# Kernel tuning notes

Hardware: AMD Instinct MI355X
Metric: run time of the kernel (lower is better)

The kernel has to match this reference:

```python
import jax, jax.numpy as jnp
import numpy as np

FP8_MAX = 448.0  # finfo(float8_e4m3fn).max
EPS = 1e-12
BLK = 128        # weight_block_size = (128, 128); activation group_size = 128


def setup_inputs() -> dict:
    key = jax.random.key(0)
    k1, k2, k3, k4 = jax.random.split(key, 4)
    B, S, H, O = 4, 4096, 2048, 2048
    x = jax.random.normal(k1, (B, S, H), dtype=jnp.float32)
    # fp8 weight: generate, round to e4m3fn grid, store as f32 (values exactly fp8-representable)
    w_raw = jax.random.normal(k2, (O, H), dtype=jnp.float32) * 0.02
    weight = w_raw.astype(jnp.float8_e4m3fn).astype(jnp.float32)
    # per-(128x128)-block weight scales
    weight_scale = jax.random.uniform(k3, (O // BLK, H // BLK), dtype=jnp.float32,
                                      minval=0.001, maxval=0.01)
    bias = jax.random.normal(k4, (O,), dtype=jnp.float32) * 0.01
    return {"x": x, "weight": weight, "weight_scale": weight_scale, "bias": bias}


def reference(x, weight, weight_scale, bias):
    B, S, H = x.shape
    O = weight.shape[0]
    J = H // BLK  # number of activation groups / weight column-blocks
    # per-token-group fp8 quantization (group_size = BLK)
    xg = x.reshape(-1, J, BLK)                                      # [M, J, BLK]
    max_abs = jnp.clip(jnp.max(jnp.abs(xg), axis=-1, keepdims=True), EPS)
    scales = FP8_MAX / max_abs                                      # [M, J, 1]
    xq = jnp.clip(xg * scales, -FP8_MAX, FP8_MAX)
    xq = xq.astype(jnp.float8_e4m3fn).astype(jnp.float32)           # fp8 round-trip
    inv_scale = 1.0 / scales                                        # stored input_scale
    # block-scaled matmul == dequantize both operands then single GEMM
    x_dq = (xq * inv_scale).reshape(-1, H)                          # [M, H]
    w_scale_full = jnp.repeat(jnp.repeat(weight_scale, BLK, axis=0), BLK, axis=1)  # [O, H]
    w_dq = weight * w_scale_full                                    # [O, H]
    y = x_dq @ w_dq.T + bias                                        # [M, O]
    return y.reshape(B, S, O)
```

## Files before the change

kernel.cpp:

```cpp
#include <hip/hip_runtime.h>
#include <cstdint>

#define FP8MAX 448.0f

typedef float f32x4 __attribute__((ext_vector_type(4)));
typedef int   i32x4 __attribute__((ext_vector_type(4)));
typedef int   i32x8 __attribute__((ext_vector_type(8)));

union frag8 { i32x8 v8; i32x4 v4[2]; };

__device__ __forceinline__ void gload_lds16(const void* g, void* l) {
  __builtin_amdgcn_global_load_lds(
      (const __attribute__((address_space(1))) unsigned int*)g,
      (__attribute__((address_space(3))) unsigned int*)l,
      16, 0, 0);
}

__global__ __launch_bounds__(256) void quant_x(const float* __restrict__ x,
                                               uint8_t* __restrict__ xq,
                                               float* __restrict__ sa) {
  const int m = blockIdx.x;
  const int t = threadIdx.x;
  const float* xr = x + (size_t)m * 2048;
  float4 v0 = ((const float4*)xr)[t * 2];
  float4 v1 = ((const float4*)xr)[t * 2 + 1];
  float amax = fmaxf(fmaxf(fmaxf(fabsf(v0.x), fabsf(v0.y)), fmaxf(fabsf(v0.z), fabsf(v0.w))),
                     fmaxf(fmaxf(fabsf(v1.x), fabsf(v1.y)), fmaxf(fabsf(v1.z), fabsf(v1.w))));
  #pragma unroll
  for (int off = 1; off < 16; off <<= 1)
    amax = fmaxf(amax, __shfl_xor(amax, off));
  amax = fmaxf(amax, 1e-12f);
  float s   = FP8MAX / amax;
  float inv = 1.0f / s;
  if ((t & 15) == 0) sa[(size_t)m * 16 + (t >> 4)] = inv;
  float q[8] = {v0.x * s, v0.y * s, v0.z * s, v0.w * s,
                v1.x * s, v1.y * s, v1.z * s, v1.w * s};
  #pragma unroll
  for (int i = 0; i < 8; ++i) q[i] = fminf(fmaxf(q[i], -FP8MAX), FP8MAX);
  union { unsigned long long u; unsigned int w[2]; } pk;
  pk.w[0] = __builtin_amdgcn_cvt_pk_fp8_f32(q[0], q[1], 0, false);
  pk.w[0] = __builtin_amdgcn_cvt_pk_fp8_f32(q[2], q[3], pk.w[0], true);
  pk.w[1] = __builtin_amdgcn_cvt_pk_fp8_f32(q[4], q[5], 0, false);
  pk.w[1] = __builtin_amdgcn_cvt_pk_fp8_f32(q[6], q[7], pk.w[1], true);
  ((unsigned long long*)(xq + (size_t)m * 2048))[t] = pk.u;
}

__global__ __launch_bounds__(256) void conv_w(const float* __restrict__ w,
                                              uint8_t* __restrict__ w8, int n8) {
  int i = blockIdx.x * 256 + threadIdx.x;
  if (i >= n8) return;
  float4 v0 = ((const float4*)w)[i * 2];
  float4 v1 = ((const float4*)w)[i * 2 + 1];
  union { unsigned long long u; unsigned int x[2]; } pk;
  pk.x[0] = __builtin_amdgcn_cvt_pk_fp8_f32(v0.x, v0.y, 0, false);
  pk.x[0] = __builtin_amdgcn_cvt_pk_fp8_f32(v0.z, v0.w, pk.x[0], true);
  pk.x[1] = __builtin_amdgcn_cvt_pk_fp8_f32(v1.x, v1.y, 0, false);
  pk.x[1] = __builtin_amdgcn_cvt_pk_fp8_f32(v1.z, v1.w, pk.x[1], true);
  ((unsigned long long*)w8)[i] = pk.u;
}

#define SAL_STRIDE 264

__global__ __launch_bounds__(512, 2) void gemm_fp8(
    const uint8_t* __restrict__ A, const uint8_t* __restrict__ Bw,
    const float* __restrict__ sa, const float* __restrict__ sb,
    const float* __restrict__ bias, float* __restrict__ out,
    int M, int N, int K) {
  const int J = K >> 7;
  const int nbn = N >> 8;
  int bid = blockIdx.x;
  int nwg = gridDim.x;
  if ((nwg & 7) == 0) {
    int cpx = nwg >> 3;
    bid = (bid & 7) * cpx + (bid >> 3);
  }
  const int bn = bid % nbn;
  const int bm = bid / nbn;
  const int t = threadIdx.x;
  const int lane = t & 63;
  const int w = t >> 6;
  const int wr = w >> 2;
  const int wc = w & 3;
  const int r16 = lane & 15;
  const int kg = lane >> 4;

  __shared__ __align__(16) uint8_t lA[2][256 * 128];
  __shared__ __align__(16) uint8_t lB[2][256 * 128];
  __shared__ __align__(16) float sal[16 * SAL_STRIDE];

  const uint8_t* gA = A + (size_t)bm * 256 * K;
  const uint8_t* gB = Bw + (size_t)bn * 256 * K;

  for (int i = t; i < 256 * 16; i += 512) {
    int row = i >> 4, j = i & 15;
    sal[j * SAL_STRIDE + row] = sa[((size_t)bm * 256 + row) * 16 + j];
  }

  const int rl = t >> 3;
  const int sg = t & 7;

  #define STAGE(ldst, gbase, h_, kt_) do {                                   \
    _Pragma("unroll")                                                        \
    for (int it_ = 0; it_ < 2; ++it_) {                                      \
      int r_ = it_ * 64 + rl;                                                \
      int gr_ = (h_) * 128 + r_;                                             \
      gload_lds16(gbase + (size_t)gr_ * K + ((kt_) << 7) +                   \
                      ((sg ^ (r_ & 7)) << 4),                                \
                  (ldst) + gr_ * 128 + sg * 16);                             \
    } } while (0)

  __syncthreads();

  STAGE(lA[0], gA, 0, 0);
  STAGE(lB[0], gB, 0, 0);
  STAGE(lA[0], gA, 1, 0);
  STAGE(lB[0], gB, 1, 0);
  STAGE(lA[1], gA, 0, 1);
  STAGE(lB[1], gB, 0, 1);

  f32x4 tot[8][4] = {};
  const f32x4 fz = {0.f, 0.f, 0.f, 0.f};
  frag8 av[4], bv[2][2];
  f32x4 scq[4];

  #define BAR1_VM8  do { asm volatile("s_waitcnt vmcnt(8)" ::: "memory");    \
                         __builtin_amdgcn_s_barrier();                       \
                         asm volatile("" ::: "memory"); } while (0)
  #define BAR1      do { __builtin_amdgcn_s_barrier();                       \
                         asm volatile("" ::: "memory"); } while (0)
  #define MID       do { asm volatile("s_waitcnt lgkmcnt(0)" ::: "memory");  \
                         __builtin_amdgcn_sched_barrier(0); } while (0)
  #define BAR2      do { __builtin_amdgcn_s_barrier();                       \
                         asm volatile("" ::: "memory"); } while (0)

  #define READ_A(mg_, buf_) do { _Pragma("unroll")                           \
    for (int i_ = 0; i_ < 4; ++i_) {                                         \
      int row_ = (mg_) * 128 + wr * 64 + i_ * 16 + r16;                      \
      const uint8_t* bp_ = &lA[buf_][row_ * 128];                            \
      int sw_ = (row_ & 7) << 4;                                             \
      av[i_].v4[0] = *(const i32x4*)(bp_ + ((kg * 32) ^ sw_));               \
      av[i_].v4[1] = *(const i32x4*)(bp_ + ((kg * 32 + 16) ^ sw_));          \
    } } while (0)

  #define READ_B(ng_, buf_) do { _Pragma("unroll")                           \
    for (int j_ = 0; j_ < 2; ++j_) {                                         \
      int row_ = (ng_) * 128 + wc * 32 + j_ * 16 + r16;                      \
      const uint8_t* bp_ = &lB[buf_][row_ * 128];                            \
      int sw_ = (row_ & 7) << 4;                                             \
      bv[ng_][j_].v4[0] = *(const i32x4*)(bp_ + ((kg * 32) ^ sw_));          \
      bv[ng_][j_].v4[1] = *(const i32x4*)(bp_ + ((kg * 32 + 16) ^ sw_));     \
    } } while (0)

  #define CALC_SC(mg_, kt_, sbj_) do { _Pragma("unroll")                     \
    for (int i_ = 0; i_ < 4; ++i_) {                                         \
      scq[i_] = (*(const f32x4*)&sal[(kt_) * SAL_STRIDE + (mg_) * 128 +      \
                                     wr * 64 + i_ * 16 + kg * 4]) * (sbj_);  \
    } } while (0)

  #define MFMA8(mg_, ng_) do {                                               \
    __builtin_amdgcn_s_setprio(1);                                           \
    _Pragma("unroll")                                                        \
    for (int i_ = 0; i_ < 4; ++i_) { _Pragma("unroll")                       \
      for (int j_ = 0; j_ < 2; ++j_) {                                       \
        f32x4 p_ = __builtin_amdgcn_mfma_scale_f32_16x16x128_f8f6f4(         \
            av[i_].v8, bv[ng_][j_].v8, fz, 0, 0, 0, 0x7f7f7f7f, 0,           \
            0x7f7f7f7f);                                                     \
        tot[(mg_) * 4 + i_][(ng_) * 2 + j_] += p_ * scq[i_];                 \
      } }                                                                    \
    __builtin_amdgcn_s_setprio(0); } while (0)

  const int KT = K >> 7;
  const int NI = KT >> 1;
  for (int i = 0; i < NI; ++i) {
    const int kt = 2 * i;
    const int kt2 = (kt + 2 < KT) ? kt + 2 : kt + 2 - KT;
    const int kt3 = (kt + 3 < KT) ? kt + 3 : kt + 3 - KT;
    const float sb0  = sb[(bn * 2 + 0) * J + kt];
    const float sb1  = sb[(bn * 2 + 1) * J + kt];
    const float sb0n = sb[(bn * 2 + 0) * J + kt + 1];
    const float sb1n = sb[(bn * 2 + 1) * J + kt + 1];
    BAR1_VM8;
    READ_A(0, 0); READ_B(0, 0); CALC_SC(0, kt, sb0);
    STAGE(lA[1], gA, 1, kt + 1); STAGE(lB[1], gB, 1, kt + 1);
    MID; MFMA8(0, 0); BAR2;
    BAR1_VM8;
    READ_B(1, 0); CALC_SC(0, kt, sb1);
    MID; MFMA8(0, 1); BAR2;
    BAR1;
    READ_A(1, 0); CALC_SC(1, kt, sb0);
    STAGE(lA[0], gA, 0, kt2);
    MID; MFMA8(1, 0); BAR2;
    BAR1;
    CALC_SC(1, kt, sb1);
    STAGE(lB[0], gB, 0, kt2);
    MID; MFMA8(1, 1); BAR2;
    BAR1_VM8;
    READ_A(0, 1); READ_B(0, 1); CALC_SC(0, kt + 1, sb0n);
    STAGE(lA[0], gA, 1, kt2); STAGE(lB[0], gB, 1, kt2);
    MID; MFMA8(0, 0); BAR2;
    BAR1_VM8;
    READ_B(1, 1); CALC_SC(0, kt + 1, sb1n);
    MID; MFMA8(0, 1); BAR2;
    BAR1;
    READ_A(1, 1); CALC_SC(1, kt + 1, sb0n);
    STAGE(lA[1], gA, 0, kt3);
    MID; MFMA8(1, 0); BAR2;
    BAR1;
    CALC_SC(1, kt + 1, sb1n);
    STAGE(lB[1], gB, 0, kt3);
    MID; MFMA8(1, 1); BAR2;
  }
  asm volatile("s_waitcnt vmcnt(0)" ::: "memory");

  #pragma unroll
  for (int ng = 0; ng < 2; ++ng) {
    float bb[2];
    #pragma unroll
    for (int j = 0; j < 2; ++j)
      bb[j] = bias[bn * 256 + ng * 128 + wc * 32 + j * 16 + r16];
    #pragma unroll
    for (int mg = 0; mg < 2; ++mg) {
      #pragma unroll
      for (int i = 0; i < 4; ++i) {
        int row0 = bm * 256 + mg * 128 + wr * 64 + i * 16 + kg * 4;
        #pragma unroll
        for (int r = 0; r < 4; ++r) {
          float* orow = out + (size_t)(row0 + r) * N + bn * 256 + ng * 128 + wc * 32;
          #pragma unroll
          for (int j = 0; j < 2; ++j)
            orow[j * 16 + r16] = tot[mg * 4 + i][ng * 2 + j][r] + bb[j];
        }
      }
    }
  }
}

extern "C" void kernel_launch(void* const* d_in, const int* in_sizes, int n_in,
                              void* d_out, int out_size, void* d_ws, size_t ws_size,
                              hipStream_t stream) {
  const float* x    = (const float*)d_in[0];
  const float* wt   = (const float*)d_in[1];
  const float* wsc  = (const float*)d_in[2];
  const float* bias = (const float*)d_in[3];
  float* out = (float*)d_out;

  const int O = in_sizes[3];
  const int H = in_sizes[1] / O;
  const int M = in_sizes[0] / H;

  uint8_t* xq = (uint8_t*)d_ws;
  uint8_t* w8 = xq + (size_t)M * H;
  float*   sa = (float*)(w8 + (size_t)O * H);

  quant_x<<<M, 256, 0, stream>>>(x, xq, sa);
  int n8 = O * H / 8;
  conv_w<<<(n8 + 255) / 256, 256, 0, stream>>>(wt, w8, n8);
  int grid = (M / 256) * (O / 256);
  gemm_fp8<<<grid, 512, 0, stream>>>(xq, w8, sa, wsc, bias, out, M, O, H);
}
```

Before: 156.0 us.

## Restructure GEMM main-loop barriers and vmcnt waits for finer-grained load tracking

Result: slower. 162.4 us (+4.2%).

```diff
diff --git a/kernel.cpp b/kernel.cpp
--- a/kernel.cpp
+++ b/kernel.cpp
@@ -59,7 +59,7 @@
   ((unsigned long long*)w8)[i] = pk.u;
 }
 
-#define SAL_STRIDE 264
+#define SAL_STRIDE 260
 
 __global__ __launch_bounds__(512, 2) void gemm_fp8(
     const uint8_t* __restrict__ A, const uint8_t* __restrict__ Bw,
@@ -99,7 +99,7 @@
   const int rl = t >> 3;
   const int sg = t & 7;
 
-  #define STAGE(ldst, gbase, h_, kt_) do {                                   \
+  #define STAGE2(ldst, gbase, h_, kt_) do {                                  \
     _Pragma("unroll")                                                        \
     for (int it_ = 0; it_ < 2; ++it_) {                                      \
       int r_ = it_ * 64 + rl;                                                \
@@ -111,27 +111,26 @@
 
   __syncthreads();
 
-  STAGE(lA[0], gA, 0, 0);
-  STAGE(lB[0], gB, 0, 0);
-  STAGE(lA[0], gA, 1, 0);
-  STAGE(lB[0], gB, 1, 0);
-  STAGE(lA[1], gA, 0, 1);
-  STAGE(lB[1], gB, 0, 1);
+  STAGE2(lA[0], gA, 0, 0);
+  STAGE2(lB[0], gB, 0, 0);
+  STAGE2(lA[0], gA, 1, 0);
+  STAGE2(lB[0], gB, 1, 0);
+  STAGE2(lA[1], gA, 0, 1);
+  STAGE2(lB[1], gB, 0, 1);
+  asm volatile("s_waitcnt vmcnt(4)" ::: "memory");
+  __builtin_amdgcn_s_barrier();
+  asm volatile("" ::: "memory");
 
   f32x4 tot[8][4] = {};
   const f32x4 fz = {0.f, 0.f, 0.f, 0.f};
   frag8 av[4], bv[2][2];
   f32x4 scq[4];
 
-  #define BAR1_VM8  do { asm volatile("s_waitcnt vmcnt(8)" ::: "memory");    \
-                         __builtin_amdgcn_s_barrier();                       \
-                         asm volatile("" ::: "memory"); } while (0)
-  #define BAR1      do { __builtin_amdgcn_s_barrier();                       \
+  #define VM(NN)    asm volatile("s_waitcnt vmcnt(" #NN ")" ::: "memory")
+  #define BARN      do { __builtin_amdgcn_s_barrier();                       \
                          asm volatile("" ::: "memory"); } while (0)
   #define MID       do { asm volatile("s_waitcnt lgkmcnt(0)" ::: "memory");  \
                          __builtin_amdgcn_sched_barrier(0); } while (0)
-  #define BAR2      do { __builtin_amdgcn_s_barrier();                       \
-                         asm volatile("" ::: "memory"); } while (0)
 
   #define READ_A(mg_, buf_) do { _Pragma("unroll")                           \
     for (int i_ = 0; i_ < 4; ++i_) {                                         \
@@ -179,36 +178,31 @@
     const float sb1  = sb[(bn * 2 + 1) * J + kt];
     const float sb0n = sb[(bn * 2 + 0) * J + kt + 1];
     const float sb1n = sb[(bn * 2 + 1) * J + kt + 1];
-    BAR1_VM8;
     READ_A(0, 0); READ_B(0, 0); CALC_SC(0, kt, sb0);
-    STAGE(lA[1], gA, 1, kt + 1); STAGE(lB[1], gB, 1, kt + 1);
-    MID; MFMA8(0, 0); BAR2;
-    BAR1_VM8;
+    STAGE2(lA[1], gA, 1, kt + 1); STAGE2(lB[1], gB, 1, kt + 1);
+    BARN; MID; MFMA8(0, 0); BARN;
     READ_B(1, 0); CALC_SC(0, kt, sb1);
-    MID; MFMA8(0, 1); BAR2;
-    BAR1;
+    BARN; MID; MFMA8(0, 1); BARN;
     READ_A(1, 0); CALC_SC(1, kt, sb0);
-    STAGE(lA[0], gA, 0, kt2);
-    MID; MFMA8(1, 0); BAR2;
-    BAR1;
+    STAGE2(lA[0], gA, 0, kt2);
+    BARN; MID; MFMA8(1, 0); BARN;
     CALC_SC(1, kt, sb1);
-    STAGE(lB[0], gB, 0, kt2);
-    MID; MFMA8(1, 1); BAR2;
-    BAR1_VM8;
+    VM(6);
+    STAGE2(lB[0], gB, 0, kt2);
+    BARN; MID; MFMA8(1, 1); BARN;
     READ_A(0, 1); READ_B(0, 1); CALC_SC(0, kt + 1, sb0n);
-    STAGE(lA[0], gA, 1, kt2); STAGE(lB[0], gB, 1, kt2);
-    MID; MFMA8(0, 0); BAR2;
-    BAR1_VM8;
+    VM(4);
+    STAGE2(lA[0], gA, 1, kt2); STAGE2(lB[0], gB, 1, kt2);
+    BARN; MID; MFMA8(0, 0); BARN;
     READ_B(1, 1); CALC_SC(0, kt + 1, sb1n);
-    MID; MFMA8(0, 1); BAR2;
-    BAR1;
+    BARN; MID; MFMA8(0, 1); BARN;
     READ_A(1, 1); CALC_SC(1, kt + 1, sb0n);
-    STAGE(lA[1], gA, 0, kt3);
-    MID; MFMA8(1, 0); BAR2;
-    BAR1;
+    STAGE2(lA[1], gA, 0, kt3);
+    BARN; MID; MFMA8(1, 0); BARN;
     CALC_SC(1, kt + 1, sb1n);
-    STAGE(lB[1], gB, 0, kt3);
-    MID; MFMA8(1, 1); BAR2;
+    VM(2);
+    STAGE2(lB[1], gB, 0, kt3);
+    BARN; MID; MFMA8(1, 1); BARN;
   }
   asm volatile("s_waitcnt vmcnt(0)" ::: "memory");
 
```
